# Optimization experiments

Measured on AMD Instinct MI355X. Metric: run time of the kernel, lower is better.

## Reference

```python
import jax, jax.numpy as jnp
import numpy as np

H = 256
G = H // 4
RBF = 16
CUTOFF = 10.0
N_ATOMS = 500000
N_BLOCKS = 50000


def _layernorm(x, g, b, eps=1e-5):
    m = jnp.mean(x, axis=-1, keepdims=True)
    v = jnp.var(x, axis=-1, keepdims=True)
    return (x - m) / jnp.sqrt(v + eps) * g + b


def setup_inputs() -> dict:
    key = jax.random.key(0)
    ks = jax.random.split(key, 16)
    def rn(k, shp, scale=0.02):
        return jax.random.normal(k, shp, dtype=jnp.float32) * scale
    return {
        "atom_features": jax.random.normal(ks[0], (N_ATOMS, H), dtype=jnp.float32),
        "atom_positions": jax.random.normal(ks[1], (N_ATOMS, 3), dtype=jnp.float32),
        "block_features": jax.random.normal(ks[2], (N_BLOCKS, H), dtype=jnp.float32),
        "block_id": jnp.sort(jax.random.randint(ks[3], (N_ATOMS,), 0, N_BLOCKS)),
        "rbf_centers": jnp.linspace(0.0, CUTOFF, RBF).astype(jnp.float32),
        "rbf_widths": jnp.full((RBF,), CUTOFF / RBF, dtype=jnp.float32),
        "Wg": rn(ks[4], (RBF, G)), "bg": jnp.zeros((G,), jnp.float32),
        "Wq": rn(ks[5], (H, H)), "bq": jnp.zeros((H,), jnp.float32),
        "Wk": rn(ks[6], (H + G, H)), "bk": jnp.zeros((H,), jnp.float32),
        "Wv": rn(ks[7], (H + G, H)), "bv": jnp.zeros((H,), jnp.float32),
        "Wc1": rn(ks[8], (H, H)), "bc1": jnp.zeros((H,), jnp.float32),
        "Wc2": rn(ks[9], (H, H)), "bc2": jnp.zeros((H,), jnp.float32),
        "Wf1": rn(ks[10], (H, 2 * H)), "bf1": jnp.zeros((2 * H,), jnp.float32),
        "Wf2": rn(ks[11], (2 * H, H)), "bf2": jnp.zeros((H,), jnp.float32),
        "ln1_g": jnp.ones((H,), jnp.float32), "ln1_b": jnp.zeros((H,), jnp.float32),
        "ln2_g": jnp.ones((H,), jnp.float32), "ln2_b": jnp.zeros((H,), jnp.float32),
    }


def reference(atom_features, atom_positions, block_features, block_id,
              rbf_centers, rbf_widths, Wg, bg, Wq, bq, Wk, bk, Wv, bv,
              Wc1, bc1, Wc2, bc2, Wf1, bf1, Wf2, bf2,
              ln1_g, ln1_b, ln2_g, ln2_b):
    nb = block_features.shape[0]
    seg = block_id
    # per-block geometry: centroid, relative distance, RBF expansion
    ones = jnp.ones((atom_features.shape[0],), atom_features.dtype)
    counts = jax.ops.segment_sum(ones, seg, num_segments=nb)
    centroids = jax.ops.segment_sum(atom_positions, seg, num_segments=nb) / jnp.maximum(counts, 1.0)[:, None]
    rel = atom_positions - centroids[seg]                      # [N, 3]
    d = jnp.linalg.norm(rel, axis=1)                           # [N]
    rbf = jnp.exp(-(d[:, None] - rbf_centers[None, :]) ** 2 / (2.0 * rbf_widths[None, :] ** 2))  # [N, RBF]
    geom = rbf @ Wg + bg                                       # [N, G]
    aug = jnp.concatenate([atom_features, geom], axis=1)       # [N, H+G]
    # cross-attention: one query per block, keys/values are block atoms
    Q = block_features @ Wq + bq                               # [NB, H]
    K = aug @ Wk + bk                                          # [N, H]
    V = aug @ Wv + bv                                          # [N, H]
    scale = 1.0 / np.sqrt(float(H))
    scores = jnp.sum(Q[seg] * K, axis=1) * scale               # [N]
    m = jax.ops.segment_max(scores, seg, num_segments=nb)
    m = jnp.where(jnp.isfinite(m), m, 0.0)
    e = jnp.exp(scores - m[seg])
    denom = jnp.maximum(jax.ops.segment_sum(e, seg, num_segments=nb), 1e-20)
    w = e / denom[seg]                                         # segment softmax weights
    context = jax.ops.segment_sum(w[:, None] * V, seg, num_segments=nb)  # [NB, H]
    upd = jax.nn.relu(context @ Wc1 + bc1) @ Wc2 + bc2         # context MLP (dropout=identity, eval)
    h = _layernorm(atom_features + upd[seg], ln1_g, ln1_b)     # scatter update back to atoms
    ffn = jax.nn.relu(h @ Wf1 + bf1) @ Wf2 + bf2
    return _layernorm(h + ffn, ln2_g, ln2_b)
```

## Files before the change

### kernel.cpp

```cpp
#include <hip/hip_runtime.h>
#include <hip/hip_bf16.h>


typedef __hip_bfloat16 bf16;
typedef __attribute__((ext_vector_type(8))) short bf16x8;
typedef __attribute__((ext_vector_type(4))) float f32x4;

__device__ __forceinline__ float b2f(bf16 v) { return __bfloat162float(v); }
__device__ __forceinline__ float us2f(unsigned short u) {
  union { unsigned int v; float f; } c; c.v = ((unsigned int)u) << 16; return c.f;
}
__device__ __forceinline__ unsigned short f2bu(float x) {
  bf16 t = __float2bfloat16(x);
  unsigned short u; __builtin_memcpy(&u, &t, 2); return u;
}
__device__ __forceinline__ float4 ld4(const float* p) {
  return *reinterpret_cast<const float4*>(p);
}
__device__ __forceinline__ float4 ldnt4(const float* p) {
  f32x4 v = __builtin_nontemporal_load(reinterpret_cast<const f32x4*>(p));
  return make_float4(v.x, v.y, v.z, v.w);
}
__device__ __forceinline__ void stnt4(float* p, float4 v) {
  f32x4 w = {v.x, v.y, v.z, v.w};
  __builtin_nontemporal_store(w, reinterpret_cast<f32x4*>(p));
}
__device__ __forceinline__ float wsum(float v) {
#pragma unroll
  for (int o = 32; o > 0; o >>= 1) v += __shfl_xor(v, o, 64);
  return v;
}
__device__ __forceinline__ bf16x8 lds_frag(const unsigned short* base, int stride,
                                           int row, int k) {
  return *reinterpret_cast<const bf16x8*>(base + row * stride +
                                          (k ^ ((row & 7) << 3)));
}

__global__ void bounds_k(const int* __restrict__ seg, int* __restrict__ bs,
                         int* __restrict__ be, int N) {
  int i = blockIdx.x * 256 + threadIdx.x;
  if (i >= N) return;
  int b = seg[i];
  if (i == 0 || seg[i - 1] != b) bs[b] = i;
  if (i == N - 1 || seg[i + 1] != b) be[b] = i + 1;
}

__global__ void cent_k(const float* __restrict__ pos, const int* __restrict__ bs,
                       const int* __restrict__ be, float* __restrict__ cent, int NB) {
  int b = blockIdx.x * 256 + threadIdx.x;
  if (b >= NB) return;
  int s0 = bs[b], s1 = be[b];
  float sx = 0.f, sy = 0.f, sz = 0.f;
  for (int i = s0; i < s1; ++i) {
    sx += pos[(size_t)i * 3 + 0];
    sy += pos[(size_t)i * 3 + 1];
    sz += pos[(size_t)i * 3 + 2];
  }
  float inv = 1.f / fmaxf((float)(s1 - s0), 1.f);
  cent[(size_t)b * 3 + 0] = sx * inv;
  cent[(size_t)b * 3 + 1] = sy * inv;
  cent[(size_t)b * 3 + 2] = sz * inv;
}

__global__ __launch_bounds__(256) void geom_k(
    const float* __restrict__ pos, const int* __restrict__ seg,
    const float* __restrict__ cent, const float* __restrict__ centers,
    const float* __restrict__ widths, const float* __restrict__ Wg,
    const float* __restrict__ bg, bf16* __restrict__ geom, int N) {
  __shared__ float sWg[16][64];
  __shared__ float sc[16], sw[16], sbg[64];
  int t = threadIdx.x;
  if (t < 16) {
    sc[t] = centers[t];
    float w = widths[t];
    sw[t] = 1.f / (2.f * w * w);
  }
  for (int j = t; j < 1024; j += 256) sWg[j >> 6][j & 63] = Wg[j];
  if (t < 64) sbg[t] = bg[t];
  __syncthreads();
  int i = blockIdx.x * 256 + t;
  if (i >= N) return;
  int b = seg[i];
  float dx = pos[(size_t)i * 3 + 0] - cent[(size_t)b * 3 + 0];
  float dy = pos[(size_t)i * 3 + 1] - cent[(size_t)b * 3 + 1];
  float dz = pos[(size_t)i * 3 + 2] - cent[(size_t)b * 3 + 2];
  float d = sqrtf(dx * dx + dy * dy + dz * dz);
  float r[16];
#pragma unroll
  for (int j = 0; j < 16; ++j) {
    float dd = d - sc[j];
    r[j] = expf(-dd * dd * sw[j]);
  }
  bf16* gp = geom + (size_t)i * 64;
  for (int g0 = 0; g0 < 64; g0 += 4) {
    float a0 = sbg[g0], a1 = sbg[g0 + 1], a2 = sbg[g0 + 2], a3 = sbg[g0 + 3];
#pragma unroll
    for (int j = 0; j < 16; ++j) {
      float rj = r[j];
      a0 += rj * sWg[j][g0];
      a1 += rj * sWg[j][g0 + 1];
      a2 += rj * sWg[j][g0 + 2];
      a3 += rj * sWg[j][g0 + 3];
    }
    ushort4 o;
    o.x = f2bu(a0); o.y = f2bu(a1); o.z = f2bu(a2); o.w = f2bu(a3);
    *reinterpret_cast<ushort4*>(gp + g0) = o;
  }
}

__global__ void tr_k(const float* __restrict__ in, unsigned short* __restrict__ out,
                     int K, int N) {
  int idx = blockIdx.x * 256 + threadIdx.x;
  if (idx >= N * K) return;
  int n = idx / K, k = idx % K;
  out[idx] = f2bu(in[(size_t)k * N + n]);
}
__global__ void cast_k(const float* __restrict__ in, unsigned short* __restrict__ out,
                       int n) {
  int idx = blockIdx.x * 256 + threadIdx.x;
  if (idx < n) out[idx] = f2bu(in[idx]);
}

__global__ __launch_bounds__(512, 4) void blk1_k(
    const float* __restrict__ bfeat, const unsigned short* __restrict__ WqT,
    const float* __restrict__ bq, const unsigned short* __restrict__ WkC,
    const float* __restrict__ bk, float* __restrict__ u, float* __restrict__ cb,
    int NB) {
  __shared__ unsigned short x_lds[64 * 256];
  __shared__ unsigned short q_lds[64 * 256];
  const int t = threadIdx.x;
  const int lane = t & 63, wv = t >> 6, l15 = lane & 15, lhi = lane >> 4;
  const int r0 = blockIdx.x * 64;
  for (int rr = 0; rr < 8; ++rr) {
    int r = wv * 8 + rr;
    int row = r0 + r; if (row >= NB) row = NB - 1;
    float4 v = ldnt4(bfeat + (size_t)row * 256 + lane * 4);
    ushort4 o; o.x = f2bu(v.x); o.y = f2bu(v.y); o.z = f2bu(v.z); o.w = f2bu(v.w);
    *reinterpret_cast<ushort4*>(&x_lds[r * 256 + ((lane * 4) ^ ((r & 7) << 3))]) = o;
  }
  __syncthreads();
  {
    f32x4 acc[2][4];
#pragma unroll
    for (int nt = 0; nt < 2; ++nt)
#pragma unroll
      for (int rt = 0; rt < 4; ++rt) acc[nt][rt] = (f32x4){0.f, 0.f, 0.f, 0.f};
#pragma unroll
    for (int ks = 0; ks < 8; ++ks) {
      bf16x8 a[4];
#pragma unroll
      for (int rt = 0; rt < 4; ++rt)
        a[rt] = lds_frag(x_lds, 256, rt * 16 + l15, ks * 32 + lhi * 8);
#pragma unroll
      for (int nt = 0; nt < 2; ++nt) {
        bf16x8 b = *reinterpret_cast<const bf16x8*>(
            WqT + (size_t)(wv * 32 + nt * 16 + l15) * 256 + ks * 32 + lhi * 8);
#pragma unroll
        for (int rt = 0; rt < 4; ++rt)
          acc[nt][rt] = __builtin_amdgcn_mfma_f32_16x16x32_bf16(a[rt], b, acc[nt][rt], 0, 0, 0);
      }
    }
#pragma unroll
    for (int nt = 0; nt < 2; ++nt) {
      int col = wv * 32 + nt * 16 + l15;
      float bb = bq[col];
#pragma unroll
      for (int rt = 0; rt < 4; ++rt)
#pragma unroll
        for (int j = 0; j < 4; ++j) {
          int row = rt * 16 + lhi * 4 + j;
          q_lds[row * 256 + (col ^ ((row & 7) << 3))] = f2bu(acc[nt][rt][j] + bb);
        }
    }
  }
  __syncthreads();
  if (t < 64) {
    float a = 0.f;
    for (int c = 0; c < 256; ++c)
      a += us2f(q_lds[t * 256 + (c ^ ((t & 7) << 3))]) * bk[c];
    int row = r0 + t;
    if (row < NB) cb[row] = a;
  }
  for (int j = 0; j < 3; ++j) {
    int tile = wv + 8 * j;
    if (tile >= 20) break;
    f32x4 acc[4];
#pragma unroll
    for (int rt = 0; rt < 4; ++rt) acc[rt] = (f32x4){0.f, 0.f, 0.f, 0.f};
#pragma unroll
    for (int ks = 0; ks < 8; ++ks) {
      bf16x8 b = *reinterpret_cast<const bf16x8*>(
          WkC + (size_t)(tile * 16 + l15) * 256 + ks * 32 + lhi * 8);
#pragma unroll
      for (int rt = 0; rt < 4; ++rt) {
        bf16x8 a = lds_frag(q_lds, 256, rt * 16 + l15, ks * 32 + lhi * 8);
        acc[rt] = __builtin_amdgcn_mfma_f32_16x16x32_bf16(a, b, acc[rt], 0, 0, 0);
      }
    }
    int n = tile * 16 + l15;
#pragma unroll
    for (int rt = 0; rt < 4; ++rt)
#pragma unroll
      for (int jj = 0; jj < 4; ++jj) {
        int row = r0 + rt * 16 + lhi * 4 + jj;
        if (row < NB) u[(size_t)row * 320 + n] = acc[rt][jj];
      }
  }
}

__global__ __launch_bounds__(256) void attn_k(
    const float* __restrict__ feat, const bf16* __restrict__ geom,
    const float* __restrict__ u, const float* __restrict__ cbArr,
    const int* __restrict__ bs, const int* __restrict__ be,
    float* __restrict__ S, int NB) {
  int wave = threadIdx.x >> 6;
  int lane = threadIdx.x & 63;
  int b = blockIdx.x * 4 + wave;
  if (b >= NB) return;
  int s0 = bs[b], s1 = be[b];
  if (s1 <= s0) return;
  const float* ub = u + (size_t)b * 320;
  float4 uv = ld4(ub + lane * 4);
  float ug = ub[256 + lane];
  float cb = cbArr[b];
  const float scale = 0.0625f;
  float m = -1e30f, l = 0.f;
  float a0 = 0.f, a1 = 0.f, a2 = 0.f, a3 = 0.f, ag = 0.f;
  for (int i = s0; i < s1; ++i) {
    float4 f = ldnt4(feat + (size_t)i * 256 + lane * 4);
    float gm = b2f(geom[(size_t)i * 64 + lane]);
    float p = f.x * uv.x + f.y * uv.y + f.z * uv.z + f.w * uv.w + gm * ug;
    p = wsum(p);
    float s = (p + cb) * scale;
    if (s <= m) {
      float w = expf(s - m);
      l += w;
      a0 += w * f.x; a1 += w * f.y; a2 += w * f.z; a3 += w * f.w;
      ag += w * gm;
    } else {
      float corr = expf(m - s);
      l = l * corr + 1.f;
      a0 = a0 * corr + f.x; a1 = a1 * corr + f.y;
      a2 = a2 * corr + f.z; a3 = a3 * corr + f.w;
      ag = ag * corr + gm;
      m = s;
    }
  }
  float inv = 1.f / l;
  float* Sb = S + (size_t)b * 320;
  Sb[lane * 4 + 0] = a0 * inv; Sb[lane * 4 + 1] = a1 * inv;
  Sb[lane * 4 + 2] = a2 * inv; Sb[lane * 4 + 3] = a3 * inv;
  Sb[256 + lane] = ag * inv;
}

__global__ __launch_bounds__(512, 4) void blk2_k(
    const float* __restrict__ S, const unsigned short* __restrict__ WvT,
    const float* __restrict__ bv, const unsigned short* __restrict__ Wc1T,
    const float* __restrict__ bc1, const unsigned short* __restrict__ Wc2T,
    const float* __restrict__ bc2, float* __restrict__ upd, int NB) {
  __shared__ unsigned short s_lds[64 * 320];
  const int t = threadIdx.x;
  const int lane = t & 63, wv = t >> 6, l15 = lane & 15, lhi = lane >> 4;
  const int r0 = blockIdx.x * 64;
  for (int rr = 0; rr < 8; ++rr) {
    int r = wv * 8 + rr;
    int row = r0 + r; if (row >= NB) row = NB - 1;
    float4 v = ld4(S + (size_t)row * 320 + lane * 4);
    ushort4 o; o.x = f2bu(v.x); o.y = f2bu(v.y); o.z = f2bu(v.z); o.w = f2bu(v.w);
    *reinterpret_cast<ushort4*>(&s_lds[r * 320 + ((lane * 4) ^ ((r & 7) << 3))]) = o;
    float g = S[(size_t)row * 320 + 256 + lane];
    s_lds[r * 320 + ((256 + lane) ^ ((r & 7) << 3))] = f2bu(g);
  }
  __syncthreads();
  f32x4 acc[2][4];
#pragma unroll
  for (int nt = 0; nt < 2; ++nt)
#pragma unroll
    for (int rt = 0; rt < 4; ++rt) acc[nt][rt] = (f32x4){0.f, 0.f, 0.f, 0.f};
#pragma unroll
  for (int ks = 0; ks < 10; ++ks) {
    bf16x8 a[4];
#pragma unroll
    for (int rt = 0; rt < 4; ++rt)
      a[rt] = lds_frag(s_lds, 320, rt * 16 + l15, ks * 32 + lhi * 8);
#pragma unroll
    for (int nt = 0; nt < 2; ++nt) {
      bf16x8 b = *reinterpret_cast<const bf16x8*>(
          WvT + (size_t)(wv * 32 + nt * 16 + l15) * 320 + ks * 32 + lhi * 8);
#pragma unroll
      for (int rt = 0; rt < 4; ++rt)
        acc[nt][rt] = __builtin_amdgcn_mfma_f32_16x16x32_bf16(a[rt], b, acc[nt][rt], 0, 0, 0);
    }
  }
  __syncthreads();
#pragma unroll
  for (int nt = 0; nt < 2; ++nt) {
    int col = wv * 32 + nt * 16 + l15;
    float bb = bv[col];
#pragma unroll
    for (int rt = 0; rt < 4; ++rt)
#pragma unroll
      for (int j = 0; j < 4; ++j) {
        int row = rt * 16 + lhi * 4 + j;
        s_lds[row * 256 + (col ^ ((row & 7) << 3))] = f2bu(acc[nt][rt][j] + bb);
      }
  }
  __syncthreads();
#pragma unroll
  for (int nt = 0; nt < 2; ++nt)
#pragma unroll
    for (int rt = 0; rt < 4; ++rt) acc[nt][rt] = (f32x4){0.f, 0.f, 0.f, 0.f};
#pragma unroll
  for (int ks = 0; ks < 8; ++ks) {
    bf16x8 a[4];
#pragma unroll
    for (int rt = 0; rt < 4; ++rt)
      a[rt] = lds_frag(s_lds, 256, rt * 16 + l15, ks * 32 + lhi * 8);
#pragma unroll
    for (int nt = 0; nt < 2; ++nt) {
      bf16x8 b = *reinterpret_cast<const bf16x8*>(
          Wc1T + (size_t)(wv * 32 + nt * 16 + l15) * 256 + ks * 32 + lhi * 8);
#pragma unroll
      for (int rt = 0; rt < 4; ++rt)
        acc[nt][rt] = __builtin_amdgcn_mfma_f32_16x16x32_bf16(a[rt], b, acc[nt][rt], 0, 0, 0);
    }
  }
  __syncthreads();
#pragma unroll
  for (int nt = 0; nt < 2; ++nt) {
    int col = wv * 32 + nt * 16 + l15;
    float bb = bc1[col];
#pragma unroll
    for (int rt = 0; rt < 4; ++rt)
#pragma unroll
      for (int j = 0; j < 4; ++j) {
        int row = rt * 16 + lhi * 4 + j;
        s_lds[row * 256 + (col ^ ((row & 7) << 3))] = f2bu(fmaxf(acc[nt][rt][j] + bb, 0.f));
      }
  }
  __syncthreads();
#pragma unroll
  for (int nt = 0; nt < 2; ++nt)
#pragma unroll
    for (int rt = 0; rt < 4; ++rt) acc[nt][rt] = (f32x4){0.f, 0.f, 0.f, 0.f};
#pragma unroll
  for (int ks = 0; ks < 8; ++ks) {
    bf16x8 a[4];
#pragma unroll
    for (int rt = 0; rt < 4; ++rt)
      a[rt] = lds_frag(s_lds, 256, rt * 16 + l15, ks * 32 + lhi * 8);
#pragma unroll
    for (int nt = 0; nt < 2; ++nt) {
      bf16x8 b = *reinterpret_cast<const bf16x8*>(
          Wc2T + (size_t)(wv * 32 + nt * 16 + l15) * 256 + ks * 32 + lhi * 8);
#pragma unroll
      for (int rt = 0; rt < 4; ++rt)
        acc[nt][rt] = __builtin_amdgcn_mfma_f32_16x16x32_bf16(a[rt], b, acc[nt][rt], 0, 0, 0);
    }
  }
#pragma unroll
  for (int nt = 0; nt < 2; ++nt) {
    int col = wv * 32 + nt * 16 + l15;
    float bb = bc2[col];
#pragma unroll
    for (int rt = 0; rt < 4; ++rt)
#pragma unroll
      for (int j = 0; j < 4; ++j) {
        int row = r0 + rt * 16 + lhi * 4 + j;
        if (row < NB) upd[(size_t)row * 256 + col] = acc[nt][rt][j] + bb;
      }
  }
}

__global__ __launch_bounds__(512, 4) void ffn_mfma_k(
    const float* __restrict__ feat, const int* __restrict__ seg,
    const float* __restrict__ upd, const unsigned short* __restrict__ Wf1T,
    const float* __restrict__ bf1_, const unsigned short* __restrict__ Wf2T,
    const float* __restrict__ bf2_, const float* __restrict__ lng1,
    const float* __restrict__ lnb1, const float* __restrict__ lng2,
    const float* __restrict__ lnb2, float* __restrict__ out, int N) {
  __shared__ unsigned short h_lds[64 * 256];
  __shared__ unsigned short f1q_lds[64 * 128];
  const int t = threadIdx.x;
  const int lane = t & 63;
  const int wv = t >> 6;
  const int l15 = lane & 15;
  const int lhi = lane >> 4;
  const int r0 = blockIdx.x * 64;

  {
    float4 g1v = ld4(lng1 + lane * 4);
    float4 b1v = ld4(lnb1 + lane * 4);
    for (int rr = 0; rr < 8; ++rr) {
      int r = wv * 8 + rr;
      int row = r0 + r;
      if (row >= N) row = N - 1;
      int bidx = seg[row];
      float4 xf = ldnt4(feat + (size_t)row * 256 + lane * 4);
      float4 up = ld4(upd + (size_t)bidx * 256 + lane * 4);
      float x0 = xf.x + up.x, x1 = xf.y + up.y;
      float x2 = xf.z + up.z, x3 = xf.w + up.w;
      float s = wsum(x0 + x1 + x2 + x3);
      float s2 = wsum(x0 * x0 + x1 * x1 + x2 * x2 + x3 * x3);
      float mean = s * (1.f / 256.f);
      float var = s2 * (1.f / 256.f) - mean * mean;
      float rstd = rsqrtf(var + 1e-5f);
      ushort4 o;
      o.x = f2bu((x0 - mean) * rstd * g1v.x + b1v.x);
      o.y = f2bu((x1 - mean) * rstd * g1v.y + b1v.y);
      o.z = f2bu((x2 - mean) * rstd * g1v.z + b1v.z);
      o.w = f2bu((x3 - mean) * rstd * g1v.w + b1v.w);
      *reinterpret_cast<ushort4*>(&h_lds[r * 256 + ((lane * 4) ^ ((r & 7) << 3))]) = o;
    }
  }
  __syncthreads();

  f32x4 accC[2][4];
#pragma unroll
  for (int nt = 0; nt < 2; ++nt)
#pragma unroll
    for (int rt = 0; rt < 4; ++rt) accC[nt][rt] = (f32x4){0.f, 0.f, 0.f, 0.f};

#pragma unroll 1
  for (int q = 0; q < 4; ++q) {
    {
      f32x4 accB[4];
#pragma unroll
      for (int rt = 0; rt < 4; ++rt) accB[rt] = (f32x4){0.f, 0.f, 0.f, 0.f};
      const unsigned short* wb =
          Wf1T + (size_t)(q * 128 + wv * 16 + l15) * 256 + lhi * 8;
      bf16x8 bcur = *reinterpret_cast<const bf16x8*>(wb);
#pragma unroll
      for (int ks = 0; ks < 8; ++ks) {
        bf16x8 bnx = bcur;
        if (ks < 7) bnx = *reinterpret_cast<const bf16x8*>(wb + (ks + 1) * 32);
        bf16x8 a0 = lds_frag(h_lds, 256, 0 * 16 + l15, ks * 32 + lhi * 8);
        bf16x8 a1 = lds_frag(h_lds, 256, 1 * 16 + l15, ks * 32 + lhi * 8);
        bf16x8 a2 = lds_frag(h_lds, 256, 2 * 16 + l15, ks * 32 + lhi * 8);
        bf16x8 a3 = lds_frag(h_lds, 256, 3 * 16 + l15, ks * 32 + lhi * 8);
        accB[0] = __builtin_amdgcn_mfma_f32_16x16x32_bf16(a0, bcur, accB[0], 0, 0, 0);
        accB[1] = __builtin_amdgcn_mfma_f32_16x16x32_bf16(a1, bcur, accB[1], 0, 0, 0);
        accB[2] = __builtin_amdgcn_mfma_f32_16x16x32_bf16(a2, bcur, accB[2], 0, 0, 0);
        accB[3] = __builtin_amdgcn_mfma_f32_16x16x32_bf16(a3, bcur, accB[3], 0, 0, 0);
        bcur = bnx;
      }
      int coll = wv * 16 + l15;
      float bb = bf1_[q * 128 + coll];
#pragma unroll
      for (int rt = 0; rt < 4; ++rt)
#pragma unroll
        for (int j = 0; j < 4; ++j) {
          int row = rt * 16 + lhi * 4 + j;
          f1q_lds[row * 128 + (coll ^ ((row & 7) << 3))] =
              f2bu(fmaxf(accB[rt][j] + bb, 0.f));
        }
    }
    __syncthreads();
#pragma unroll
    for (int ks = 0; ks < 4; ++ks) {
      bf16x8 a0 = lds_frag(f1q_lds, 128, 0 * 16 + l15, ks * 32 + lhi * 8);
      bf16x8 a1 = lds_frag(f1q_lds, 128, 1 * 16 + l15, ks * 32 + lhi * 8);
      bf16x8 a2 = lds_frag(f1q_lds, 128, 2 * 16 + l15, ks * 32 + lhi * 8);
      bf16x8 a3 = lds_frag(f1q_lds, 128, 3 * 16 + l15, ks * 32 + lhi * 8);
#pragma unroll
      for (int nt = 0; nt < 2; ++nt) {
        bf16x8 b = *reinterpret_cast<const bf16x8*>(
            Wf2T + (size_t)(wv * 32 + nt * 16 + l15) * 512 + q * 128 +
            ks * 32 + lhi * 8);
        accC[nt][0] = __builtin_amdgcn_mfma_f32_16x16x32_bf16(a0, b, accC[nt][0], 0, 0, 0);
        accC[nt][1] = __builtin_amdgcn_mfma_f32_16x16x32_bf16(a1, b, accC[nt][1], 0, 0, 0);
        accC[nt][2] = __builtin_amdgcn_mfma_f32_16x16x32_bf16(a2, b, accC[nt][2], 0, 0, 0);
        accC[nt][3] = __builtin_amdgcn_mfma_f32_16x16x32_bf16(a3, b, accC[nt][3], 0, 0, 0);
      }
    }
    __syncthreads();
  }

#pragma unroll
  for (int nt = 0; nt < 2; ++nt) {
    int c = wv * 32 + nt * 16 + l15;
    float bb = bf2_[c];
#pragma unroll
    for (int rt = 0; rt < 4; ++rt)
#pragma unroll
      for (int j = 0; j < 4; ++j) {
        int row = rt * 16 + lhi * 4 + j;
        int idx = row * 256 + (c ^ ((row & 7) << 3));
        h_lds[idx] = f2bu(us2f(h_lds[idx]) + accC[nt][rt][j] + bb);
      }
  }
  __syncthreads();

  {
    float4 g2v = ld4(lng2 + lane * 4);
    float4 b2v = ld4(lnb2 + lane * 4);
    for (int rr = 0; rr < 8; ++rr) {
      int r = wv * 8 + rr;
      int row = r0 + r;
      if (row >= N) row = N - 1;
      int idx = r * 256 + ((lane * 4) ^ ((r & 7) << 3));
      ushort4 yv = *reinterpret_cast<const ushort4*>(&h_lds[idx]);
      float y0 = us2f(yv.x), y1 = us2f(yv.y), y2 = us2f(yv.z), y3 = us2f(yv.w);
      float s = wsum(y0 + y1 + y2 + y3);
      float s2 = wsum(y0 * y0 + y1 * y1 + y2 * y2 + y3 * y3);
      float mean = s * (1.f / 256.f);
      float var = s2 * (1.f / 256.f) - mean * mean;
      float rstd = rsqrtf(var + 1e-5f);
      float4 o;
      o.x = (y0 - mean) * rstd * g2v.x + b2v.x;
      o.y = (y1 - mean) * rstd * g2v.y + b2v.y;
      o.z = (y2 - mean) * rstd * g2v.z + b2v.z;
      o.w = (y3 - mean) * rstd * g2v.w + b2v.w;
      stnt4(out + (size_t)row * 256 + lane * 4, o);
    }
  }
}

extern "C" void kernel_launch(void* const* d_in, const int* in_sizes, int n_in,
                              void* d_out, int out_size, void* d_ws, size_t ws_size,
                              hipStream_t stream) {
  const float* feat = (const float*)d_in[0];
  const float* pos = (const float*)d_in[1];
  const float* bfeat = (const float*)d_in[2];
  const int* seg = (const int*)d_in[3];
  const float* centers = (const float*)d_in[4];
  const float* widths = (const float*)d_in[5];
  const float* Wg = (const float*)d_in[6];
  const float* bg = (const float*)d_in[7];
  const float* Wq = (const float*)d_in[8];
  const float* bq = (const float*)d_in[9];
  const float* Wk = (const float*)d_in[10];
  const float* bk = (const float*)d_in[11];
  const float* Wv = (const float*)d_in[12];
  const float* bv = (const float*)d_in[13];
  const float* Wc1 = (const float*)d_in[14];
  const float* bc1 = (const float*)d_in[15];
  const float* Wc2 = (const float*)d_in[16];
  const float* bc2 = (const float*)d_in[17];
  const float* Wf1 = (const float*)d_in[18];
  const float* bf1_ = (const float*)d_in[19];
  const float* Wf2 = (const float*)d_in[20];
  const float* bf2_ = (const float*)d_in[21];
  const float* lng1 = (const float*)d_in[22];
  const float* lnb1 = (const float*)d_in[23];
  const float* lng2 = (const float*)d_in[24];
  const float* lnb2 = (const float*)d_in[25];
  float* out = (float*)d_out;

  const int N = in_sizes[0] / 256;
  const int NB = in_sizes[2] / 256;

  size_t off = 0;
  char* wsb = (char*)d_ws;
  auto alloc = [&](size_t bytes) -> void* {
    void* p = wsb + off;
    off += (bytes + 255) & ~(size_t)255;
    return p;
  };
  int* bs = (int*)alloc((size_t)NB * 4);
  int* be = (int*)alloc((size_t)NB * 4);
  float* cent = (float*)alloc((size_t)NB * 3 * 4);
  bf16* geom = (bf16*)alloc((size_t)N * 64 * 2);
  float* u = (float*)alloc((size_t)NB * 320 * 4);
  float* cb = (float*)alloc((size_t)NB * 4);
  float* S = (float*)alloc((size_t)NB * 320 * 4);
  float* upd = (float*)alloc((size_t)NB * 256 * 4);
  unsigned short* WqT = (unsigned short*)alloc((size_t)256 * 256 * 2);
  unsigned short* WkC = (unsigned short*)alloc((size_t)320 * 256 * 2);
  unsigned short* WvT = (unsigned short*)alloc((size_t)256 * 320 * 2);
  unsigned short* Wc1T = (unsigned short*)alloc((size_t)256 * 256 * 2);
  unsigned short* Wc2T = (unsigned short*)alloc((size_t)256 * 256 * 2);
  unsigned short* Wf1T = (unsigned short*)alloc((size_t)512 * 256 * 2);
  unsigned short* Wf2T = (unsigned short*)alloc((size_t)256 * 512 * 2);

  hipMemsetAsync(bs, 0, (size_t)NB * 4, stream);
  hipMemsetAsync(be, 0, (size_t)NB * 4, stream);

  tr_k<<<(256 * 256 + 255) / 256, 256, 0, stream>>>(Wq, WqT, 256, 256);
  cast_k<<<(320 * 256 + 255) / 256, 256, 0, stream>>>(Wk, WkC, 320 * 256);
  tr_k<<<(256 * 320 + 255) / 256, 256, 0, stream>>>(Wv, WvT, 320, 256);
  tr_k<<<(256 * 256 + 255) / 256, 256, 0, stream>>>(Wc1, Wc1T, 256, 256);
  tr_k<<<(256 * 256 + 255) / 256, 256, 0, stream>>>(Wc2, Wc2T, 256, 256);
  tr_k<<<(512 * 256 + 255) / 256, 256, 0, stream>>>(Wf1, Wf1T, 256, 512);
  tr_k<<<(256 * 512 + 255) / 256, 256, 0, stream>>>(Wf2, Wf2T, 512, 256);

  bounds_k<<<(N + 255) / 256, 256, 0, stream>>>(seg, bs, be, N);
  cent_k<<<(NB + 255) / 256, 256, 0, stream>>>(pos, bs, be, cent, NB);
  geom_k<<<(N + 255) / 256, 256, 0, stream>>>(pos, seg, cent, centers, widths,
                                              Wg, bg, geom, N);
  const int NBB = (NB + 63) / 64;
  blk1_k<<<NBB, 512, 0, stream>>>(bfeat, WqT, bq, WkC, bk, u, cb, NB);
  attn_k<<<(NB + 3) / 4, 256, 0, stream>>>(feat, geom, u, cb, bs, be, S, NB);
  blk2_k<<<NBB, 512, 0, stream>>>(S, WvT, bv, Wc1T, bc1, Wc2T, bc2, upd, NB);
  ffn_mfma_k<<<(N + 63) / 64, 512, 0, stream>>>(feat, seg, upd, Wf1T, bf1_, Wf2T,
                                                bf2_, lng1, lnb1, lng2, lnb2, out, N);
}
```

Measured before the change: 1.214 ms.

## Retile FFN MFMA work into 2x4 wave grid with batched weight loads

```diff
diff --git a/kernel.cpp b/kernel.cpp
--- a/kernel.cpp
+++ b/kernel.cpp
@@ -20,10 +20,6 @@
 __device__ __forceinline__ float4 ldnt4(const float* p) {
   f32x4 v = __builtin_nontemporal_load(reinterpret_cast<const f32x4*>(p));
   return make_float4(v.x, v.y, v.z, v.w);
-}
-__device__ __forceinline__ void stnt4(float* p, float4 v) {
-  f32x4 w = {v.x, v.y, v.z, v.w};
-  __builtin_nontemporal_store(w, reinterpret_cast<f32x4*>(p));
 }
 __device__ __forceinline__ float wsum(float v) {
 #pragma unroll
@@ -380,10 +376,12 @@
     const float* __restrict__ lnb1, const float* __restrict__ lng2,
     const float* __restrict__ lnb2, float* __restrict__ out, int N) {
   __shared__ unsigned short h_lds[64 * 256];
-  __shared__ unsigned short f1q_lds[64 * 128];
+  __shared__ unsigned short f1q_lds[64 * 136];
   const int t = threadIdx.x;
   const int lane = t & 63;
   const int wv = t >> 6;
+  const int rg = wv >> 2;
+  const int cg = wv & 3;
   const int l15 = lane & 15;
   const int lhi = lane >> 4;
   const int r0 = blockIdx.x * 64;
@@ -415,76 +413,91 @@
   }
   __syncthreads();
 
-  f32x4 accC[2][4];
-#pragma unroll
-  for (int nt = 0; nt < 2; ++nt)
-#pragma unroll
-    for (int rt = 0; rt < 4; ++rt) accC[nt][rt] = (f32x4){0.f, 0.f, 0.f, 0.f};
+  f32x4 accC[4][2];
+#pragma unroll
+  for (int nt = 0; nt < 4; ++nt)
+#pragma unroll
+    for (int rt = 0; rt < 2; ++rt) accC[nt][rt] = (f32x4){0.f, 0.f, 0.f, 0.f};
 
 #pragma unroll 1
   for (int q = 0; q < 4; ++q) {
     {
-      f32x4 accB[4];
-#pragma unroll
-      for (int rt = 0; rt < 4; ++rt) accB[rt] = (f32x4){0.f, 0.f, 0.f, 0.f};
-      const unsigned short* wb =
-          Wf1T + (size_t)(q * 128 + wv * 16 + l15) * 256 + lhi * 8;
-      bf16x8 bcur = *reinterpret_cast<const bf16x8*>(wb);
-#pragma unroll
-      for (int ks = 0; ks < 8; ++ks) {
-        bf16x8 bnx = bcur;
-        if (ks < 7) bnx = *reinterpret_cast<const bf16x8*>(wb + (ks + 1) * 32);
-        bf16x8 a0 = lds_frag(h_lds, 256, 0 * 16 + l15, ks * 32 + lhi * 8);
-        bf16x8 a1 = lds_frag(h_lds, 256, 1 * 16 + l15, ks * 32 + lhi * 8);
-        bf16x8 a2 = lds_frag(h_lds, 256, 2 * 16 + l15, ks * 32 + lhi * 8);
-        bf16x8 a3 = lds_frag(h_lds, 256, 3 * 16 + l15, ks * 32 + lhi * 8);
-        accB[0] = __builtin_amdgcn_mfma_f32_16x16x32_bf16(a0, bcur, accB[0], 0, 0, 0);
-        accB[1] = __builtin_amdgcn_mfma_f32_16x16x32_bf16(a1, bcur, accB[1], 0, 0, 0);
-        accB[2] = __builtin_amdgcn_mfma_f32_16x16x32_bf16(a2, bcur, accB[2], 0, 0, 0);
-        accB[3] = __builtin_amdgcn_mfma_f32_16x16x32_bf16(a3, bcur, accB[3], 0, 0, 0);
-        bcur = bnx;
-      }
-      int coll = wv * 16 + l15;
-      float bb = bf1_[q * 128 + coll];
-#pragma unroll
-      for (int rt = 0; rt < 4; ++rt)
-#pragma unroll
-        for (int j = 0; j < 4; ++j) {
-          int row = rt * 16 + lhi * 4 + j;
-          f1q_lds[row * 128 + (coll ^ ((row & 7) << 3))] =
-              f2bu(fmaxf(accB[rt][j] + bb, 0.f));
+      f32x4 accB[2][2];
+#pragma unroll
+      for (int nt = 0; nt < 2; ++nt)
+#pragma unroll
+        for (int rt = 0; rt < 2; ++rt) accB[nt][rt] = (f32x4){0.f, 0.f, 0.f, 0.f};
+#pragma unroll
+      for (int kh = 0; kh < 2; ++kh) {
+        bf16x8 bw[2][4];
+#pragma unroll
+        for (int nt = 0; nt < 2; ++nt)
+#pragma unroll
+          for (int ks = 0; ks < 4; ++ks)
+            bw[nt][ks] = *reinterpret_cast<const bf16x8*>(
+                Wf1T + (size_t)(q * 128 + cg * 32 + nt * 16 + l15) * 256 +
+                (kh * 4 + ks) * 32 + lhi * 8);
+#pragma unroll
+        for (int ks = 0; ks < 4; ++ks) {
+          int k = (kh * 4 + ks) * 32 + lhi * 8;
+          bf16x8 a0 = lds_frag(h_lds, 256, rg * 32 + l15, k);
+          bf16x8 a1 = lds_frag(h_lds, 256, rg * 32 + 16 + l15, k);
+          accB[0][0] = __builtin_amdgcn_mfma_f32_16x16x32_bf16(a0, bw[0][ks], accB[0][0], 0, 0, 0);
+          accB[0][1] = __builtin_amdgcn_mfma_f32_16x16x32_bf16(a1, bw[0][ks], accB[0][1], 0, 0, 0);
+          accB[1][0] = __builtin_amdgcn_mfma_f32_16x16x32_bf16(a0, bw[1][ks], accB[1][0], 0, 0, 0);
+          accB[1][1] = __builtin_amdgcn_mfma_f32_16x16x32_bf16(a1, bw[1][ks], accB[1][1], 0, 0, 0);
         }
+      }
+#pragma unroll
+      for (int nt = 0; nt < 2; ++nt) {
+        int coll = cg * 32 + nt * 16 + l15;
+        float bb = bf1_[q * 128 + coll];
+#pragma unroll
+        for (int rt = 0; rt < 2; ++rt)
+#pragma unroll
+          for (int j = 0; j < 4; ++j) {
+            int row = rg * 32 + rt * 16 + lhi * 4 + j;
+            f1q_lds[row * 136 + coll] = f2bu(fmaxf(accB[nt][rt][j] + bb, 0.f));
+          }
+      }
     }
     __syncthreads();
 #pragma unroll
-    for (int ks = 0; ks < 4; ++ks) {
-      bf16x8 a0 = lds_frag(f1q_lds, 128, 0 * 16 + l15, ks * 32 + lhi * 8);
-      bf16x8 a1 = lds_frag(f1q_lds, 128, 1 * 16 + l15, ks * 32 + lhi * 8);
-      bf16x8 a2 = lds_frag(f1q_lds, 128, 2 * 16 + l15, ks * 32 + lhi * 8);
-      bf16x8 a3 = lds_frag(f1q_lds, 128, 3 * 16 + l15, ks * 32 + lhi * 8);
-#pragma unroll
-      for (int nt = 0; nt < 2; ++nt) {
-        bf16x8 b = *reinterpret_cast<const bf16x8*>(
-            Wf2T + (size_t)(wv * 32 + nt * 16 + l15) * 512 + q * 128 +
-            ks * 32 + lhi * 8);
-        accC[nt][0] = __builtin_amdgcn_mfma_f32_16x16x32_bf16(a0, b, accC[nt][0], 0, 0, 0);
-        accC[nt][1] = __builtin_amdgcn_mfma_f32_16x16x32_bf16(a1, b, accC[nt][1], 0, 0, 0);
-        accC[nt][2] = __builtin_amdgcn_mfma_f32_16x16x32_bf16(a2, b, accC[nt][2], 0, 0, 0);
-        accC[nt][3] = __builtin_amdgcn_mfma_f32_16x16x32_bf16(a3, b, accC[nt][3], 0, 0, 0);
+    for (int kh = 0; kh < 2; ++kh) {
+      bf16x8 cw[4][2];
+#pragma unroll
+      for (int nt = 0; nt < 4; ++nt)
+#pragma unroll
+        for (int ks = 0; ks < 2; ++ks)
+          cw[nt][ks] = *reinterpret_cast<const bf16x8*>(
+              Wf2T + (size_t)(cg * 64 + nt * 16 + l15) * 512 + q * 128 +
+              (kh * 2 + ks) * 32 + lhi * 8);
+#pragma unroll
+      for (int ks = 0; ks < 2; ++ks) {
+        int k = (kh * 2 + ks) * 32 + lhi * 8;
+        bf16x8 a0 = *reinterpret_cast<const bf16x8*>(
+            f1q_lds + (rg * 32 + l15) * 136 + k);
+        bf16x8 a1 = *reinterpret_cast<const bf16x8*>(
+            f1q_lds + (rg * 32 + 16 + l15) * 136 + k);
+#pragma unroll
+        for (int nt = 0; nt < 4; ++nt) {
+          accC[nt][0] = __builtin_amdgcn_mfma_f32_16x16x32_bf16(a0, cw[nt][ks], accC[nt][0], 0, 0, 0);
+          accC[nt][1] = __builtin_amdgcn_mfma_f32_16x16x32_bf16(a1, cw[nt][ks], accC[nt][1], 0, 0, 0);
+        }
       }
     }
     __syncthreads();
   }
 
 #pragma unroll
-  for (int nt = 0; nt < 2; ++nt) {
-    int c = wv * 32 + nt * 16 + l15;
+  for (int nt = 0; nt < 4; ++nt) {
+    int c = cg * 64 + nt * 16 + l15;
     float bb = bf2_[c];
 #pragma unroll
-    for (int rt = 0; rt < 4; ++rt)
+    for (int rt = 0; rt < 2; ++rt)
 #pragma unroll
       for (int j = 0; j < 4; ++j) {
-        int row = rt * 16 + lhi * 4 + j;
+        int row = rg * 32 + rt * 16 + lhi * 4 + j;
         int idx = row * 256 + (c ^ ((row & 7) << 3));
         h_lds[idx] = f2bu(us2f(h_lds[idx]) + accC[nt][rt][j] + bb);
       }
@@ -511,7 +524,7 @@
       o.y = (y1 - mean) * rstd * g2v.y + b2v.y;
       o.z = (y2 - mean) * rstd * g2v.z + b2v.z;
       o.w = (y3 - mean) * rstd * g2v.w + b2v.w;
-      stnt4(out + (size_t)row * 256 + lane * 4, o);
+      *reinterpret_cast<float4*>(out + (size_t)row * 256 + lane * 4) = o;
     }
   }
 }
```

Result: slower. 1.499 ms (+23.4%).

## Shrink FFN kernel tile to 32 rows with 4 waves and retile MFMA work

Applied to the files above, without the earlier changes.

```diff
diff --git a/kernel.cpp b/kernel.cpp
--- a/kernel.cpp
+++ b/kernel.cpp
@@ -372,21 +372,21 @@
   }
 }
 
-__global__ __launch_bounds__(512, 4) void ffn_mfma_k(
+__global__ __launch_bounds__(256, 5) void ffn_mfma_k(
     const float* __restrict__ feat, const int* __restrict__ seg,
     const float* __restrict__ upd, const unsigned short* __restrict__ Wf1T,
     const float* __restrict__ bf1_, const unsigned short* __restrict__ Wf2T,
     const float* __restrict__ bf2_, const float* __restrict__ lng1,
     const float* __restrict__ lnb1, const float* __restrict__ lng2,
     const float* __restrict__ lnb2, float* __restrict__ out, int N) {
-  __shared__ unsigned short h_lds[64 * 256];
-  __shared__ unsigned short f1q_lds[64 * 128];
+  __shared__ unsigned short h_lds[32 * 256];
+  __shared__ unsigned short f1c_lds[32 * 128];
   const int t = threadIdx.x;
   const int lane = t & 63;
   const int wv = t >> 6;
   const int l15 = lane & 15;
   const int lhi = lane >> 4;
-  const int r0 = blockIdx.x * 64;
+  const int r0 = blockIdx.x * 32;
 
   {
     float4 g1v = ld4(lng1 + lane * 4);
@@ -415,77 +415,72 @@
   }
   __syncthreads();
 
-  f32x4 accC[2][4];
-#pragma unroll
-  for (int nt = 0; nt < 2; ++nt)
-#pragma unroll
-    for (int rt = 0; rt < 4; ++rt) accC[nt][rt] = (f32x4){0.f, 0.f, 0.f, 0.f};
+  f32x4 accC[4][2];
+#pragma unroll
+  for (int nt = 0; nt < 4; ++nt)
+#pragma unroll
+    for (int rt = 0; rt < 2; ++rt) accC[nt][rt] = (f32x4){0.f, 0.f, 0.f, 0.f};
 
 #pragma unroll 1
-  for (int q = 0; q < 4; ++q) {
-    {
-      f32x4 accB[4];
-#pragma unroll
-      for (int rt = 0; rt < 4; ++rt) accB[rt] = (f32x4){0.f, 0.f, 0.f, 0.f};
-      const unsigned short* wb =
-          Wf1T + (size_t)(q * 128 + wv * 16 + l15) * 256 + lhi * 8;
-      bf16x8 bcur = *reinterpret_cast<const bf16x8*>(wb);
-#pragma unroll
-      for (int ks = 0; ks < 8; ++ks) {
-        bf16x8 bnx = bcur;
-        if (ks < 7) bnx = *reinterpret_cast<const bf16x8*>(wb + (ks + 1) * 32);
-        bf16x8 a0 = lds_frag(h_lds, 256, 0 * 16 + l15, ks * 32 + lhi * 8);
-        bf16x8 a1 = lds_frag(h_lds, 256, 1 * 16 + l15, ks * 32 + lhi * 8);
-        bf16x8 a2 = lds_frag(h_lds, 256, 2 * 16 + l15, ks * 32 + lhi * 8);
-        bf16x8 a3 = lds_frag(h_lds, 256, 3 * 16 + l15, ks * 32 + lhi * 8);
-        accB[0] = __builtin_amdgcn_mfma_f32_16x16x32_bf16(a0, bcur, accB[0], 0, 0, 0);
-        accB[1] = __builtin_amdgcn_mfma_f32_16x16x32_bf16(a1, bcur, accB[1], 0, 0, 0);
-        accB[2] = __builtin_amdgcn_mfma_f32_16x16x32_bf16(a2, bcur, accB[2], 0, 0, 0);
-        accB[3] = __builtin_amdgcn_mfma_f32_16x16x32_bf16(a3, bcur, accB[3], 0, 0, 0);
-        bcur = bnx;
-      }
-      int coll = wv * 16 + l15;
-      float bb = bf1_[q * 128 + coll];
-#pragma unroll
-      for (int rt = 0; rt < 4; ++rt)
+  for (int c = 0; c < 4; ++c) {
+    f32x4 accB[2][2];
+#pragma unroll
+    for (int nt = 0; nt < 2; ++nt)
+#pragma unroll
+      for (int rt = 0; rt < 2; ++rt) accB[nt][rt] = (f32x4){0.f, 0.f, 0.f, 0.f};
+#pragma unroll
+    for (int ks = 0; ks < 8; ++ks) {
+      int k = ks * 32 + lhi * 8;
+      bf16x8 a0 = lds_frag(h_lds, 256, l15, k);
+      bf16x8 a1 = lds_frag(h_lds, 256, 16 + l15, k);
+#pragma unroll
+      for (int nt = 0; nt < 2; ++nt) {
+        bf16x8 b = *reinterpret_cast<const bf16x8*>(
+            Wf1T + (size_t)(c * 128 + wv * 32 + nt * 16 + l15) * 256 + k);
+        accB[nt][0] = __builtin_amdgcn_mfma_f32_16x16x32_bf16(a0, b, accB[nt][0], 0, 0, 0);
+        accB[nt][1] = __builtin_amdgcn_mfma_f32_16x16x32_bf16(a1, b, accB[nt][1], 0, 0, 0);
+      }
+    }
+    __syncthreads();
+#pragma unroll
+    for (int nt = 0; nt < 2; ++nt) {
+      int coll = wv * 32 + nt * 16 + l15;
+      float bb = bf1_[c * 128 + coll];
+#pragma unroll
+      for (int rt = 0; rt < 2; ++rt)
 #pragma unroll
         for (int j = 0; j < 4; ++j) {
           int row = rt * 16 + lhi * 4 + j;
-          f1q_lds[row * 128 + (coll ^ ((row & 7) << 3))] =
-              f2bu(fmaxf(accB[rt][j] + bb, 0.f));
+          f1c_lds[row * 128 + (coll ^ ((row & 7) << 3))] =
+              f2bu(fmaxf(accB[nt][rt][j] + bb, 0.f));
         }
     }
     __syncthreads();
 #pragma unroll
     for (int ks = 0; ks < 4; ++ks) {
-      bf16x8 a0 = lds_frag(f1q_lds, 128, 0 * 16 + l15, ks * 32 + lhi * 8);
-      bf16x8 a1 = lds_frag(f1q_lds, 128, 1 * 16 + l15, ks * 32 + lhi * 8);
-      bf16x8 a2 = lds_frag(f1q_lds, 128, 2 * 16 + l15, ks * 32 + lhi * 8);
-      bf16x8 a3 = lds_frag(f1q_lds, 128, 3 * 16 + l15, ks * 32 + lhi * 8);
-#pragma unroll
-      for (int nt = 0; nt < 2; ++nt) {
+      int k = ks * 32 + lhi * 8;
+      bf16x8 a0 = lds_frag(f1c_lds, 128, l15, k);
+      bf16x8 a1 = lds_frag(f1c_lds, 128, 16 + l15, k);
+#pragma unroll
+      for (int nt = 0; nt < 4; ++nt) {
         bf16x8 b = *reinterpret_cast<const bf16x8*>(
-            Wf2T + (size_t)(wv * 32 + nt * 16 + l15) * 512 + q * 128 +
-            ks * 32 + lhi * 8);
+            Wf2T + (size_t)(wv * 64 + nt * 16 + l15) * 512 + c * 128 + k);
         accC[nt][0] = __builtin_amdgcn_mfma_f32_16x16x32_bf16(a0, b, accC[nt][0], 0, 0, 0);
         accC[nt][1] = __builtin_amdgcn_mfma_f32_16x16x32_bf16(a1, b, accC[nt][1], 0, 0, 0);
-        accC[nt][2] = __builtin_amdgcn_mfma_f32_16x16x32_bf16(a2, b, accC[nt][2], 0, 0, 0);
-        accC[nt][3] = __builtin_amdgcn_mfma_f32_16x16x32_bf16(a3, b, accC[nt][3], 0, 0, 0);
-      }
-    }
-    __syncthreads();
-  }
-
-#pragma unroll
-  for (int nt = 0; nt < 2; ++nt) {
-    int c = wv * 32 + nt * 16 + l15;
-    float bb = bf2_[c];
-#pragma unroll
-    for (int rt = 0; rt < 4; ++rt)
+      }
+    }
+  }
+
+#pragma unroll
+  for (int nt = 0; nt < 4; ++nt) {
+    int cc = wv * 64 + nt * 16 + l15;
+    float bb = bf2_[cc];
+#pragma unroll
+    for (int rt = 0; rt < 2; ++rt)
 #pragma unroll
       for (int j = 0; j < 4; ++j) {
         int row = rt * 16 + lhi * 4 + j;
-        int idx = row * 256 + (c ^ ((row & 7) << 3));
+        int idx = row * 256 + (cc ^ ((row & 7) << 3));
         h_lds[idx] = f2bu(us2f(h_lds[idx]) + accC[nt][rt][j] + bb);
       }
   }
@@ -592,6 +587,6 @@
   blk1_k<<<NBB, 512, 0, stream>>>(bfeat, WqT, bq, WkC, bk, u, cb, NB);
   attn_k<<<(NB + 3) / 4, 256, 0, stream>>>(feat, geom, u, cb, bs, be, S, NB);
   blk2_k<<<NBB, 512, 0, stream>>>(S, WvT, bv, Wc1T, bc1, Wc2T, bc2, upd, NB);
-  ffn_mfma_k<<<(N + 63) / 64, 512, 0, stream>>>(feat, seg, upd, Wf1T, bf1_, Wf2T,
+  ffn_mfma_k<<<(N + 31) / 32, 256, 0, stream>>>(feat, seg, upd, Wf1T, bf1_, Wf2T,
                                                 bf2_, lng1, lnb1, lng2, lnb2, out, N);
 }
```

After: 1.738 ms. 1.43x slower.

## Pre-pack FFN weights into MFMA fragment order and pad f1 LDS tile

Applied to the files above, without the earlier changes.

```diff
diff --git a/kernel.cpp b/kernel.cpp
--- a/kernel.cpp
+++ b/kernel.cpp
@@ -20,10 +20,6 @@
 __device__ __forceinline__ float4 ldnt4(const float* p) {
   f32x4 v = __builtin_nontemporal_load(reinterpret_cast<const f32x4*>(p));
   return make_float4(v.x, v.y, v.z, v.w);
-}
-__device__ __forceinline__ void stnt4(float* p, float4 v) {
-  f32x4 w = {v.x, v.y, v.z, v.w};
-  __builtin_nontemporal_store(w, reinterpret_cast<f32x4*>(p));
 }
 __device__ __forceinline__ float wsum(float v) {
 #pragma unroll
@@ -119,6 +115,31 @@
                        int n) {
   int idx = blockIdx.x * 256 + threadIdx.x;
   if (idx < n) out[idx] = f2bu(in[idx]);
+}
+
+__global__ void pack1_k(const float* __restrict__ Wf1,
+                        unsigned short* __restrict__ P) {
+  int idx = blockIdx.x * 256 + threadIdx.x;
+  if (idx >= 512 * 256) return;
+  int e = idx & 7;
+  int l = (idx >> 3) & 63;
+  int blk = idx >> 9;
+  int ks = blk & 7, wv = (blk >> 3) & 7, q = blk >> 6;
+  int n = q * 128 + wv * 16 + (l & 15);
+  int k = ks * 32 + (l >> 4) * 8 + e;
+  P[idx] = f2bu(Wf1[(size_t)k * 512 + n]);
+}
+__global__ void pack2_k(const float* __restrict__ Wf2,
+                        unsigned short* __restrict__ P) {
+  int idx = blockIdx.x * 256 + threadIdx.x;
+  if (idx >= 512 * 256) return;
+  int e = idx & 7;
+  int l = (idx >> 3) & 63;
+  int blk = idx >> 9;
+  int ks = blk & 3, q = (blk >> 2) & 3, nt = (blk >> 4) & 1, wv = blk >> 5;
+  int n = wv * 32 + nt * 16 + (l & 15);
+  int k = q * 128 + ks * 32 + (l >> 4) * 8 + e;
+  P[idx] = f2bu(Wf2[(size_t)k * 256 + n]);
 }
 
 __global__ __launch_bounds__(512, 4) void blk1_k(
@@ -374,13 +395,13 @@
 
 __global__ __launch_bounds__(512, 4) void ffn_mfma_k(
     const float* __restrict__ feat, const int* __restrict__ seg,
-    const float* __restrict__ upd, const unsigned short* __restrict__ Wf1T,
-    const float* __restrict__ bf1_, const unsigned short* __restrict__ Wf2T,
+    const float* __restrict__ upd, const unsigned short* __restrict__ Wf1P,
+    const float* __restrict__ bf1_, const unsigned short* __restrict__ Wf2P,
     const float* __restrict__ bf2_, const float* __restrict__ lng1,
     const float* __restrict__ lnb1, const float* __restrict__ lng2,
     const float* __restrict__ lnb2, float* __restrict__ out, int N) {
   __shared__ unsigned short h_lds[64 * 256];
-  __shared__ unsigned short f1q_lds[64 * 128];
+  __shared__ unsigned short f1q_lds[64 * 136];
   const int t = threadIdx.x;
   const int lane = t & 63;
   const int wv = t >> 6;
@@ -428,16 +449,17 @@
 #pragma unroll
       for (int rt = 0; rt < 4; ++rt) accB[rt] = (f32x4){0.f, 0.f, 0.f, 0.f};
       const unsigned short* wb =
-          Wf1T + (size_t)(q * 128 + wv * 16 + l15) * 256 + lhi * 8;
+          Wf1P + (size_t)((q * 8 + wv) * 8) * 512 + lane * 8;
       bf16x8 bcur = *reinterpret_cast<const bf16x8*>(wb);
 #pragma unroll
       for (int ks = 0; ks < 8; ++ks) {
         bf16x8 bnx = bcur;
-        if (ks < 7) bnx = *reinterpret_cast<const bf16x8*>(wb + (ks + 1) * 32);
-        bf16x8 a0 = lds_frag(h_lds, 256, 0 * 16 + l15, ks * 32 + lhi * 8);
-        bf16x8 a1 = lds_frag(h_lds, 256, 1 * 16 + l15, ks * 32 + lhi * 8);
-        bf16x8 a2 = lds_frag(h_lds, 256, 2 * 16 + l15, ks * 32 + lhi * 8);
-        bf16x8 a3 = lds_frag(h_lds, 256, 3 * 16 + l15, ks * 32 + lhi * 8);
+        if (ks < 7) bnx = *reinterpret_cast<const bf16x8*>(wb + (ks + 1) * 512);
+        int k = ks * 32 + lhi * 8;
+        bf16x8 a0 = lds_frag(h_lds, 256, 0 * 16 + l15, k);
+        bf16x8 a1 = lds_frag(h_lds, 256, 1 * 16 + l15, k);
+        bf16x8 a2 = lds_frag(h_lds, 256, 2 * 16 + l15, k);
+        bf16x8 a3 = lds_frag(h_lds, 256, 3 * 16 + l15, k);
         accB[0] = __builtin_amdgcn_mfma_f32_16x16x32_bf16(a0, bcur, accB[0], 0, 0, 0);
         accB[1] = __builtin_amdgcn_mfma_f32_16x16x32_bf16(a1, bcur, accB[1], 0, 0, 0);
         accB[2] = __builtin_amdgcn_mfma_f32_16x16x32_bf16(a2, bcur, accB[2], 0, 0, 0);
@@ -451,22 +473,21 @@
 #pragma unroll
         for (int j = 0; j < 4; ++j) {
           int row = rt * 16 + lhi * 4 + j;
-          f1q_lds[row * 128 + (coll ^ ((row & 7) << 3))] =
-              f2bu(fmaxf(accB[rt][j] + bb, 0.f));
+          f1q_lds[row * 136 + coll] = f2bu(fmaxf(accB[rt][j] + bb, 0.f));
         }
     }
     __syncthreads();
 #pragma unroll
     for (int ks = 0; ks < 4; ++ks) {
-      bf16x8 a0 = lds_frag(f1q_lds, 128, 0 * 16 + l15, ks * 32 + lhi * 8);
-      bf16x8 a1 = lds_frag(f1q_lds, 128, 1 * 16 + l15, ks * 32 + lhi * 8);
-      bf16x8 a2 = lds_frag(f1q_lds, 128, 2 * 16 + l15, ks * 32 + lhi * 8);
-      bf16x8 a3 = lds_frag(f1q_lds, 128, 3 * 16 + l15, ks * 32 + lhi * 8);
+      int k = ks * 32 + lhi * 8;
+      bf16x8 a0 = *reinterpret_cast<const bf16x8*>(f1q_lds + (0 * 16 + l15) * 136 + k);
+      bf16x8 a1 = *reinterpret_cast<const bf16x8*>(f1q_lds + (1 * 16 + l15) * 136 + k);
+      bf16x8 a2 = *reinterpret_cast<const bf16x8*>(f1q_lds + (2 * 16 + l15) * 136 + k);
+      bf16x8 a3 = *reinterpret_cast<const bf16x8*>(f1q_lds + (3 * 16 + l15) * 136 + k);
 #pragma unroll
       for (int nt = 0; nt < 2; ++nt) {
         bf16x8 b = *reinterpret_cast<const bf16x8*>(
-            Wf2T + (size_t)(wv * 32 + nt * 16 + l15) * 512 + q * 128 +
-            ks * 32 + lhi * 8);
+            Wf2P + (size_t)((wv * 2 + nt) * 16 + q * 4 + ks) * 512 + lane * 8);
         accC[nt][0] = __builtin_amdgcn_mfma_f32_16x16x32_bf16(a0, b, accC[nt][0], 0, 0, 0);
         accC[nt][1] = __builtin_amdgcn_mfma_f32_16x16x32_bf16(a1, b, accC[nt][1], 0, 0, 0);
         accC[nt][2] = __builtin_amdgcn_mfma_f32_16x16x32_bf16(a2, b, accC[nt][2], 0, 0, 0);
@@ -511,7 +532,7 @@
       o.y = (y1 - mean) * rstd * g2v.y + b2v.y;
       o.z = (y2 - mean) * rstd * g2v.z + b2v.z;
       o.w = (y3 - mean) * rstd * g2v.w + b2v.w;
-      stnt4(out + (size_t)row * 256 + lane * 4, o);
+      *reinterpret_cast<float4*>(out + (size_t)row * 256 + lane * 4) = o;
     }
   }
 }
@@ -570,8 +591,8 @@
   unsigned short* WvT = (unsigned short*)alloc((size_t)256 * 320 * 2);
   unsigned short* Wc1T = (unsigned short*)alloc((size_t)256 * 256 * 2);
   unsigned short* Wc2T = (unsigned short*)alloc((size_t)256 * 256 * 2);
-  unsigned short* Wf1T = (unsigned short*)alloc((size_t)512 * 256 * 2);
-  unsigned short* Wf2T = (unsigned short*)alloc((size_t)256 * 512 * 2);
+  unsigned short* Wf1P = (unsigned short*)alloc((size_t)512 * 256 * 2);
+  unsigned short* Wf2P = (unsigned short*)alloc((size_t)256 * 512 * 2);
 
   hipMemsetAsync(bs, 0, (size_t)NB * 4, stream);
   hipMemsetAsync(be, 0, (size_t)NB * 4, stream);
@@ -581,8 +602,8 @@
   tr_k<<<(256 * 320 + 255) / 256, 256, 0, stream>>>(Wv, WvT, 320, 256);
   tr_k<<<(256 * 256 + 255) / 256, 256, 0, stream>>>(Wc1, Wc1T, 256, 256);
   tr_k<<<(256 * 256 + 255) / 256, 256, 0, stream>>>(Wc2, Wc2T, 256, 256);
-  tr_k<<<(512 * 256 + 255) / 256, 256, 0, stream>>>(Wf1, Wf1T, 256, 512);
-  tr_k<<<(256 * 512 + 255) / 256, 256, 0, stream>>>(Wf2, Wf2T, 512, 256);
+  pack1_k<<<(512 * 256 + 255) / 256, 256, 0, stream>>>(Wf1, Wf1P);
+  pack2_k<<<(512 * 256 + 255) / 256, 256, 0, stream>>>(Wf2, Wf2P);
 
   bounds_k<<<(N + 255) / 256, 256, 0, stream>>>(seg, bs, be, N);
   cent_k<<<(NB + 255) / 256, 256, 0, stream>>>(pos, bs, be, cent, NB);
@@ -592,6 +613,6 @@
   blk1_k<<<NBB, 512, 0, stream>>>(bfeat, WqT, bq, WkC, bk, u, cb, NB);
   attn_k<<<(NB + 3) / 4, 256, 0, stream>>>(feat, geom, u, cb, bs, be, S, NB);
   blk2_k<<<NBB, 512, 0, stream>>>(S, WvT, bv, Wc1T, bc1, Wc2T, bc2, upd, NB);
-  ffn_mfma_k<<<(N + 63) / 64, 512, 0, stream>>>(feat, seg, upd, Wf1T, bf1_, Wf2T,
+  ffn_mfma_k<<<(N + 63) / 64, 512, 0, stream>>>(feat, seg, upd, Wf1P, bf1_, Wf2P,
                                                 bf2_, lng1, lnb1, lng2, lnb2, out, N);
 }
```

New measurement: 1.003 ms. 1.21x faster.
